# Kernel tuning notes

Hardware: AMD Instinct MI355X
Metric: run time of the kernel (lower is better)

Reference implementation:

```python
import jax, jax.numpy as jnp
import numpy as np

TEMPERATURE = 8.0  # sqrt(d_k), d_k = 64

def setup_inputs() -> dict:
    key = jax.random.key(0)
    kq, kk, kv = jax.random.split(key, 3)
    B, S, D = 16, 4096, 64
    Q = jax.random.normal(kq, (B, S, D), dtype=jnp.float32)
    K = jax.random.normal(kk, (B, S, D), dtype=jnp.float32)
    V = jax.random.normal(kv, (B, S, D), dtype=jnp.float32)
    return {"Q": Q, "K": K, "V": V}

def reference(Q, K, V):
    # scores: [B, S, S]
    scores = jnp.einsum('bqd,bkd->bqk', Q, K) / TEMPERATURE
    attn = jax.nn.softmax(scores, axis=-1)
    # dropout(p=0.1) is identity in eval mode; omitted for deterministic reference
    x = jnp.einsum('bqk,bkd->bqd', attn, V)  # [B, S, D]
    return (x, attn)
```

## Files before the change

### kernel.cpp

```cpp
#include <hip/hip_runtime.h>

#define S 4096
#define D 64
#define NB 16

typedef _Float16 half8 __attribute__((ext_vector_type(8)));
typedef _Float16 half4 __attribute__((ext_vector_type(4)));
typedef float f32x4 __attribute__((ext_vector_type(4)));

__global__ void cvt_qk(const float* __restrict__ Q, const float* __restrict__ K,
                       _Float16* __restrict__ Qh, _Float16* __restrict__ Kh, int n) {
  int i = blockIdx.x * blockDim.x + threadIdx.x;
  int stride = gridDim.x * blockDim.x;
  for (; i < n; i += stride) {
    Qh[i] = (_Float16)(Q[i] * 0.125f);
    Kh[i] = (_Float16)(K[i]);
  }
}

__global__ void cvt_vt(const float* __restrict__ V, _Float16* __restrict__ Vt) {
  __shared__ float tile[64][65];
  int b = blockIdx.x >> 6;
  int s0 = (blockIdx.x & 63) * 64;
  const float* vb = V + ((size_t)b * S) * D;
  for (int i = threadIdx.x; i < 64 * 64; i += 256) {
    int sl = i >> 6, d = i & 63;
    tile[sl][d] = vb[(size_t)(s0 + sl) * D + d];
  }
  __syncthreads();
  _Float16* vtb = Vt + ((size_t)b * D) * S;
  for (int i = threadIdx.x; i < 64 * 64; i += 256) {
    int dl = i >> 6, sl = i & 63;
    vtb[(size_t)dl * S + s0 + sl] = (_Float16)tile[sl][dl];
  }
}

__global__ __launch_bounds__(512, 2) void attn_pv(
    const _Float16* __restrict__ Qh, const _Float16* __restrict__ Kh,
    const _Float16* __restrict__ Vt, float* __restrict__ X, float* __restrict__ Lsum) {
  const int tid = threadIdx.x;
  const int w = tid >> 6;
  const int l = tid & 63;
  const int l15 = l & 15;
  const int lq = l >> 4;
  const int r4 = lq * 4;
  const int bx = blockIdx.x;
  const int b = bx >> 8;
  const int m0 = (bx & 255) * 16;

  const _Float16* qb = Qh + ((size_t)b * S + m0) * D;
  const _Float16* kb = Kh + ((size_t)b * S) * D;
  const _Float16* vtb = Vt + ((size_t)b * D) * S;

  __shared__ float lred[8][16];
  __shared__ __align__(16) char ubuf[8][4224];

  half8 qf0 = *(const half8*)(qb + (size_t)l15 * D + lq * 8);
  half8 qf1 = *(const half8*)(qb + (size_t)l15 * D + 32 + lq * 8);

  const int nbase = w * 512;
  _Float16(*st)[72] = (_Float16(*)[72])(ubuf[w]);

  float vsum[4] = {0.f, 0.f, 0.f, 0.f};
  f32x4 xacc[4];
#pragma unroll
  for (int fd = 0; fd < 4; ++fd) xacc[fd] = (f32x4){0.f, 0.f, 0.f, 0.f};

#pragma unroll
  for (int c = 0; c < 8; ++c) {
#pragma unroll
    for (int ff = 0; ff < 4; ++ff) {
      const _Float16* kp = kb + (size_t)(nbase + (c * 4 + ff) * 16 + l15) * D + lq * 8;
      half8 kf0 = *(const half8*)(kp);
      half8 kf1 = *(const half8*)(kp + 32);
      f32x4 a = (f32x4){0.f, 0.f, 0.f, 0.f};
      a = __builtin_amdgcn_mfma_f32_16x16x32_f16(qf0, kf0, a, 0, 0, 0);
      a = __builtin_amdgcn_mfma_f32_16x16x32_f16(qf1, kf1, a, 0, 0, 0);
#pragma unroll
      for (int j = 0; j < 4; ++j) {
        float p = __expf(a[j]);
        vsum[j] += p;
        st[r4 + j][ff * 16 + l15] = (_Float16)p;
      }
    }
    asm volatile("" ::: "memory");
#pragma unroll
    for (int kh = 0; kh < 2; ++kh) {
      half8 af = *(const half8*)&st[l15][kh * 32 + lq * 8];
#pragma unroll
      for (int fd = 0; fd < 4; ++fd) {
        half8 bf = *(const half8*)(vtb + (size_t)(fd * 16 + l15) * S +
                                   nbase + c * 64 + kh * 32 + lq * 8);
        xacc[fd] = __builtin_amdgcn_mfma_f32_16x16x32_f16(af, bf, xacc[fd], 0, 0, 0);
      }
    }
    asm volatile("" ::: "memory");
  }

#pragma unroll
  for (int off = 1; off < 16; off <<= 1)
#pragma unroll
    for (int j = 0; j < 4; ++j) vsum[j] += __shfl_xor(vsum[j], off, 64);
  if (l15 == 0) {
#pragma unroll
    for (int j = 0; j < 4; ++j) lred[w][r4 + j] = vsum[j];
  }
  __syncthreads();

  if (tid < 16) {
    float s = 0.f;
#pragma unroll
    for (int ww = 0; ww < 8; ++ww) s += lred[ww][tid];
    Lsum[(size_t)b * S + m0 + tid] = __logf(s);
  }

  float rinvX[4];
#pragma unroll
  for (int j = 0; j < 4; ++j) {
    float s = 0.f;
#pragma unroll
    for (int ww = 0; ww < 8; ++ww) s += lred[ww][r4 + j];
    rinvX[j] = 1.0f / s;
  }

  float (*xr)[66] = (float(*)[66])(ubuf[w]);
#pragma unroll
  for (int fd = 0; fd < 4; ++fd)
#pragma unroll
    for (int j = 0; j < 4; ++j)
      xr[r4 + j][fd * 16 + l15] = xacc[fd][j] * rinvX[j];
  __syncthreads();
  float* xrow = X + ((size_t)b * S + m0) * D;
#pragma unroll
  for (int o = tid; o < 16 * 64; o += 512) {
    int r = o >> 6, d = o & 63;
    float s = 0.f;
#pragma unroll
    for (int ww = 0; ww < 8; ++ww) s += ((const float(*)[66])(ubuf[ww]))[r][d];
    xrow[(size_t)r * D + d] = s;
  }
}

__global__ __launch_bounds__(512, 4) void attn_store(
    const _Float16* __restrict__ Qh, const _Float16* __restrict__ Kh,
    const float* __restrict__ Lsum, float* __restrict__ Aout) {
  const int tid = threadIdx.x;
  const int w = tid >> 6;
  const int l = tid & 63;
  const int l15 = l & 15;
  const int lq = l >> 4;
  const int r4 = lq * 4;
  const int bx = blockIdx.x;
  const int b = bx >> 8;
  const int m0 = (bx & 255) * 16;

  const _Float16* qb = Qh + ((size_t)b * S + m0) * D;
  const _Float16* kb = Kh + ((size_t)b * S) * D;

  __shared__ __align__(16) _Float16 stg[8][16][72];

  half8 qf0 = *(const half8*)(qb + (size_t)l15 * D + lq * 8);
  half8 qf1 = *(const half8*)(qb + (size_t)l15 * D + 32 + lq * 8);

  float ls[4];
#pragma unroll
  for (int j = 0; j < 4; ++j) ls[j] = Lsum[(size_t)b * S + m0 + r4 + j];

  const int nbase = w * 512;
  _Float16(*st)[72] = stg[w];
  float* arow = Aout + ((size_t)b * S + m0) * S + nbase;

#pragma unroll
  for (int c = 0; c < 8; ++c) {
#pragma unroll
    for (int ff = 0; ff < 4; ++ff) {
      const _Float16* kp = kb + (size_t)(nbase + (c * 4 + ff) * 16 + l15) * D + lq * 8;
      half8 kf0 = *(const half8*)(kp);
      half8 kf1 = *(const half8*)(kp + 32);
      f32x4 a = (f32x4){0.f, 0.f, 0.f, 0.f};
      a = __builtin_amdgcn_mfma_f32_16x16x32_f16(qf0, kf0, a, 0, 0, 0);
      a = __builtin_amdgcn_mfma_f32_16x16x32_f16(qf1, kf1, a, 0, 0, 0);
#pragma unroll
      for (int j = 0; j < 4; ++j)
        st[r4 + j][ff * 16 + l15] = (_Float16)__expf(a[j] - ls[j]);
    }
    asm volatile("" ::: "memory");
#pragma unroll
    for (int i = 0; i < 4; ++i) {
      int r = lq + i * 4;
      half4 t = *(const half4*)&st[r][l15 * 4];
      f32x4 o;
#pragma unroll
      for (int q = 0; q < 4; ++q) o[q] = (float)t[q];
      *(f32x4*)(arow + (size_t)r * S + c * 64 + l15 * 4) = o;
    }
    asm volatile("" ::: "memory");
  }
}

extern "C" void kernel_launch(void* const* d_in, const int* in_sizes, int n_in,
                              void* d_out, int out_size, void* d_ws, size_t ws_size,
                              hipStream_t stream) {
  const float* Q = (const float*)d_in[0];
  const float* K = (const float*)d_in[1];
  const float* V = (const float*)d_in[2];
  float* X = (float*)d_out;
  float* A = X + (size_t)NB * S * D;
  _Float16* Qh = (_Float16*)d_ws;
  _Float16* Kh = Qh + (size_t)NB * S * D;
  _Float16* Vt = Kh + (size_t)NB * S * D;
  float* Lsum = (float*)(Vt + (size_t)NB * S * D);
  int n = NB * S * D;
  cvt_qk<<<2048, 256, 0, stream>>>(Q, K, Qh, Kh, n);
  cvt_vt<<<NB * 64, 256, 0, stream>>>(V, Vt);
  attn_pv<<<NB * 256, 512, 0, stream>>>(Qh, Kh, Vt, X, Lsum);
  attn_store<<<NB * 256, 512, 0, stream>>>(Qh, Kh, Lsum, A);
}
```

Before: 857.4 us.

## Swap MFMA operand order to drop LDS staging of probabilities

QK^T MFMA operands are swapped so each lane holds four consecutive key columns for one query row. In attn_store this lets each lane write its exponentiated scores straight to global as a float4, removing the LDS staging round trip and the fp16 quantisation of the stored attention. In attn_pv the P fragments are rearranged with cross-lane shuffles instead of LDS writes and reads, and the row-sum reduction is simplified. The cost is many more shuffle instructions, and global stores in attn_store become 16-byte pieces spread across 16 rows per instruction.

```diff
diff --git a/kernel.cpp b/kernel.cpp
--- a/kernel.cpp
+++ b/kernel.cpp
@@ -5,8 +5,9 @@
 #define NB 16
 
 typedef _Float16 half8 __attribute__((ext_vector_type(8)));
-typedef _Float16 half4 __attribute__((ext_vector_type(4)));
+typedef _Float16 half2v __attribute__((ext_vector_type(2)));
 typedef float f32x4 __attribute__((ext_vector_type(4)));
+typedef int int4v __attribute__((ext_vector_type(4)));
 
 __global__ void cvt_qk(const float* __restrict__ Q, const float* __restrict__ K,
                        _Float16* __restrict__ Qh, _Float16* __restrict__ Kh, int n) {
@@ -53,58 +54,61 @@
   const _Float16* vtb = Vt + ((size_t)b * D) * S;
 
   __shared__ float lred[8][16];
-  __shared__ __align__(16) char ubuf[8][4224];
+  __shared__ __align__(16) float xred[8][16][66];
 
   half8 qf0 = *(const half8*)(qb + (size_t)l15 * D + lq * 8);
   half8 qf1 = *(const half8*)(qb + (size_t)l15 * D + 32 + lq * 8);
 
   const int nbase = w * 512;
-  _Float16(*st)[72] = (_Float16(*)[72])(ubuf[w]);
-
-  float vsum[4] = {0.f, 0.f, 0.f, 0.f};
+  const int srcA = (lq & 1) * 32 + l15;
+  const int srcB = srcA + 16;
+  const bool hi = (lq & 2) != 0;
+
+  float vsum = 0.f;
   f32x4 xacc[4];
 #pragma unroll
   for (int fd = 0; fd < 4; ++fd) xacc[fd] = (f32x4){0.f, 0.f, 0.f, 0.f};
 
 #pragma unroll
   for (int c = 0; c < 8; ++c) {
-#pragma unroll
-    for (int ff = 0; ff < 4; ++ff) {
-      const _Float16* kp = kb + (size_t)(nbase + (c * 4 + ff) * 16 + l15) * D + lq * 8;
+    int dw[4][2];
+#pragma unroll
+    for (int f = 0; f < 4; ++f) {
+      const _Float16* kp = kb + (size_t)(nbase + c * 64 + f * 16 + l15) * D + lq * 8;
       half8 kf0 = *(const half8*)(kp);
       half8 kf1 = *(const half8*)(kp + 32);
       f32x4 a = (f32x4){0.f, 0.f, 0.f, 0.f};
-      a = __builtin_amdgcn_mfma_f32_16x16x32_f16(qf0, kf0, a, 0, 0, 0);
-      a = __builtin_amdgcn_mfma_f32_16x16x32_f16(qf1, kf1, a, 0, 0, 0);
-#pragma unroll
-      for (int j = 0; j < 4; ++j) {
-        float p = __expf(a[j]);
-        vsum[j] += p;
-        st[r4 + j][ff * 16 + l15] = (_Float16)p;
-      }
+      a = __builtin_amdgcn_mfma_f32_16x16x32_f16(kf0, qf0, a, 0, 0, 0);
+      a = __builtin_amdgcn_mfma_f32_16x16x32_f16(kf1, qf1, a, 0, 0, 0);
+      float p0 = __expf(a[0]), p1 = __expf(a[1]);
+      float p2 = __expf(a[2]), p3 = __expf(a[3]);
+      vsum += (p0 + p1) + (p2 + p3);
+      half2v h01 = {(_Float16)p0, (_Float16)p1};
+      half2v h23 = {(_Float16)p2, (_Float16)p3};
+      dw[f][0] = __builtin_bit_cast(int, h01);
+      dw[f][1] = __builtin_bit_cast(int, h23);
     }
-    asm volatile("" ::: "memory");
-#pragma unroll
-    for (int kh = 0; kh < 2; ++kh) {
-      half8 af = *(const half8*)&st[l15][kh * 32 + lq * 8];
+#pragma unroll
+    for (int w2 = 0; w2 < 2; ++w2) {
+      const int f0 = 2 * w2, f1 = 2 * w2 + 1;
+      int yA0 = __shfl(dw[f0][0], srcA, 64), yA1 = __shfl(dw[f0][1], srcA, 64);
+      int yB0 = __shfl(dw[f0][0], srcB, 64), yB1 = __shfl(dw[f0][1], srcB, 64);
+      int xA0 = __shfl(dw[f1][0], srcA, 64), xA1 = __shfl(dw[f1][1], srcA, 64);
+      int xB0 = __shfl(dw[f1][0], srcB, 64), xB1 = __shfl(dw[f1][1], srcB, 64);
+      int4v ai = {hi ? xA0 : yA0, hi ? xA1 : yA1, hi ? xB0 : yB0, hi ? xB1 : yB1};
+      half8 af = __builtin_bit_cast(half8, ai);
 #pragma unroll
       for (int fd = 0; fd < 4; ++fd) {
         half8 bf = *(const half8*)(vtb + (size_t)(fd * 16 + l15) * S +
-                                   nbase + c * 64 + kh * 32 + lq * 8);
+                                   nbase + c * 64 + w2 * 32 + lq * 8);
         xacc[fd] = __builtin_amdgcn_mfma_f32_16x16x32_f16(af, bf, xacc[fd], 0, 0, 0);
       }
     }
-    asm volatile("" ::: "memory");
-  }
-
-#pragma unroll
-  for (int off = 1; off < 16; off <<= 1)
-#pragma unroll
-    for (int j = 0; j < 4; ++j) vsum[j] += __shfl_xor(vsum[j], off, 64);
-  if (l15 == 0) {
-#pragma unroll
-    for (int j = 0; j < 4; ++j) lred[w][r4 + j] = vsum[j];
-  }
+  }
+
+  vsum += __shfl_xor(vsum, 16, 64);
+  vsum += __shfl_xor(vsum, 32, 64);
+  if (l < 16) lred[w][l] = vsum;
   __syncthreads();
 
   if (tid < 16) {
@@ -123,12 +127,11 @@
     rinvX[j] = 1.0f / s;
   }
 
-  float (*xr)[66] = (float(*)[66])(ubuf[w]);
 #pragma unroll
   for (int fd = 0; fd < 4; ++fd)
 #pragma unroll
     for (int j = 0; j < 4; ++j)
-      xr[r4 + j][fd * 16 + l15] = xacc[fd][j] * rinvX[j];
+      xred[w][r4 + j][fd * 16 + l15] = xacc[fd][j] * rinvX[j];
   __syncthreads();
   float* xrow = X + ((size_t)b * S + m0) * D;
 #pragma unroll
@@ -136,7 +139,7 @@
     int r = o >> 6, d = o & 63;
     float s = 0.f;
 #pragma unroll
-    for (int ww = 0; ww < 8; ++ww) s += ((const float(*)[66])(ubuf[ww]))[r][d];
+    for (int ww = 0; ww < 8; ++ww) s += xred[ww][r][d];
     xrow[(size_t)r * D + d] = s;
   }
 }
@@ -157,44 +160,28 @@
   const _Float16* qb = Qh + ((size_t)b * S + m0) * D;
   const _Float16* kb = Kh + ((size_t)b * S) * D;
 
-  __shared__ __align__(16) _Float16 stg[8][16][72];
-
   half8 qf0 = *(const half8*)(qb + (size_t)l15 * D + lq * 8);
   half8 qf1 = *(const half8*)(qb + (size_t)l15 * D + 32 + lq * 8);
 
-  float ls[4];
-#pragma unroll
-  for (int j = 0; j < 4; ++j) ls[j] = Lsum[(size_t)b * S + m0 + r4 + j];
-
+  const float ls = Lsum[(size_t)b * S + m0 + l15];
   const int nbase = w * 512;
-  _Float16(*st)[72] = stg[w];
-  float* arow = Aout + ((size_t)b * S + m0) * S + nbase;
+  float* arow = Aout + ((size_t)(b * S + m0 + l15)) * S + nbase + r4;
 
 #pragma unroll
   for (int c = 0; c < 8; ++c) {
 #pragma unroll
-    for (int ff = 0; ff < 4; ++ff) {
-      const _Float16* kp = kb + (size_t)(nbase + (c * 4 + ff) * 16 + l15) * D + lq * 8;
+    for (int f = 0; f < 4; ++f) {
+      const _Float16* kp = kb + (size_t)(nbase + c * 64 + f * 16 + l15) * D + lq * 8;
       half8 kf0 = *(const half8*)(kp);
       half8 kf1 = *(const half8*)(kp + 32);
       f32x4 a = (f32x4){0.f, 0.f, 0.f, 0.f};
-      a = __builtin_amdgcn_mfma_f32_16x16x32_f16(qf0, kf0, a, 0, 0, 0);
-      a = __builtin_amdgcn_mfma_f32_16x16x32_f16(qf1, kf1, a, 0, 0, 0);
-#pragma unroll
-      for (int j = 0; j < 4; ++j)
-        st[r4 + j][ff * 16 + l15] = (_Float16)__expf(a[j] - ls[j]);
+      a = __builtin_amdgcn_mfma_f32_16x16x32_f16(kf0, qf0, a, 0, 0, 0);
+      a = __builtin_amdgcn_mfma_f32_16x16x32_f16(kf1, qf1, a, 0, 0, 0);
+      f32x4 o;
+#pragma unroll
+      for (int j = 0; j < 4; ++j) o[j] = __expf(a[j] - ls);
+      *(f32x4*)(arow + c * 64 + f * 16) = o;
     }
-    asm volatile("" ::: "memory");
-#pragma unroll
-    for (int i = 0; i < 4; ++i) {
-      int r = lq + i * 4;
-      half4 t = *(const half4*)&st[r][l15 * 4];
-      f32x4 o;
-#pragma unroll
-      for (int q = 0; q < 4; ++q) o[q] = (float)t[q];
-      *(f32x4*)(arow + (size_t)r * S + c * 64 + l15 * 4) = o;
-    }
-    asm volatile("" ::: "memory");
   }
 }
 
```

After: 947.4 us. +10.5%, slower.
